# Optimization experiments

Hardware: AMD Instinct MI355X
Metric: run time of the kernel (lower is better)

Reference implementation:

```python
import jax, jax.numpy as jnp
import numpy as np


def setup_inputs() -> dict:
    key = jax.random.key(0)
    k1, k2, k3, k4 = jax.random.split(key, 4)
    N, F, E = 131072, 512, 256
    x = jax.random.normal(k1, (N, F), dtype=jnp.float32)
    W = jax.random.normal(k2, (E, F), dtype=jnp.float32) * 0.05  # stacked weak-classifier weights
    b = jax.random.normal(k3, (E,), dtype=jnp.float32) * 0.05
    alphas = jax.random.normal(k4, (E,), dtype=jnp.float32)
    return {"x": x, "W": W, "b": b, "alphas": alphas}


def reference(x, W, b, alphas):
    # Fused version of the per-estimator Python loop:
    # per estimator e: pred_e = round(sigmoid(x @ W[e] + b[e])) in {0,1}
    logits = jnp.einsum('nf,ef->ne', x, W) + b              # [N, E]
    preds = jnp.round(jax.nn.sigmoid(logits))               # [N, E], half-to-even like torch.round
    # original casts each (alpha * pred) term to long (trunc toward zero) before accumulating
    terms = jnp.trunc(alphas[None, :] * preds)              # [N, E]
    acc = jnp.sum(terms, axis=1)                            # [N]
    return jnp.sign(acc)
```

## Files before the change

### kernel.cpp

```cpp
#include <hip/hip_runtime.h>
#include <math.h>


#define F_DIM 512
#define BM    128
#define BK    32
#define NTMAX 8
#define KPAD  40
#define TAU   1e-3f

typedef float f32x4  __attribute__((ext_vector_type(4)));
typedef short bf16x8 __attribute__((ext_vector_type(8)));
typedef unsigned short u16x4 __attribute__((ext_vector_type(4)));

__device__ inline unsigned short bf16_rne(float v) {
    unsigned u = __float_as_uint(v);
    u += 0x7FFFu + ((u >> 16) & 1u);
    return (unsigned short)(u >> 16);
}
__device__ inline float bf16_to_f32(unsigned short h) {
    return __uint_as_float(((unsigned)h) << 16);
}

__device__ __attribute__((noinline)) bool exact_pred(const float* __restrict__ xr,
                                                     const float* __restrict__ wr,
                                                     float bv) {
    double s0 = 0.0, s1 = 0.0, s2 = 0.0, s3 = 0.0;
    for (int k = 0; k < F_DIM; k += 4) {
        s0 = fma((double)xr[k + 0], (double)wr[k + 0], s0);
        s1 = fma((double)xr[k + 1], (double)wr[k + 1], s1);
        s2 = fma((double)xr[k + 2], (double)wr[k + 2], s2);
        s3 = fma((double)xr[k + 3], (double)wr[k + 3], s3);
    }
    double s = ((s0 + s1) + (s2 + s3)) + (double)bv;
    return s > 0.0;
}

__global__ __launch_bounds__(256, 3)
void ada_mfma(const float* __restrict__ x, const float* __restrict__ W,
              const float* __restrict__ bias, const float* __restrict__ alphas,
              float* __restrict__ out) {
    __shared__ unsigned short xs_hi[BM][KPAD], xs_lo[BM][KPAD];
    __shared__ unsigned short wh[128][KPAD],  wl[128][KPAD];
    __shared__ int   se[272];
    __shared__ float st[272];
    __shared__ float sb[272];
    __shared__ int   wcnt[4];

    const int tid = threadIdx.x;
    const int n0  = blockIdx.x * BM;

    se[tid] = 0; st[tid] = 0.0f; sb[tid] = 0.0f;
    if (tid < 16) { se[256 + tid] = 0; st[256 + tid] = 0.0f; sb[256 + tid] = 0.0f; }
    __syncthreads();
    const float t = truncf(alphas[tid]);
    const bool flag = (t != 0.0f);
    const unsigned long long m64 = __ballot(flag);
    const int lane = tid & 63, wvi = tid >> 6;
    if (lane == 0) wcnt[wvi] = __popcll(m64);
    __syncthreads();
    int off = 0;
    #pragma unroll
    for (int w = 0; w < 4; ++w) if (w < wvi) off += wcnt[w];
    const int M = wcnt[0] + wcnt[1] + wcnt[2] + wcnt[3];
    if (flag) {
        const int slot = off + __popcll(m64 & ((1ull << lane) - 1ull));
        se[slot] = tid; st[slot] = t; sb[slot] = bias[tid];
    }
    __syncthreads();

    const int sr   = tid >> 3;
    const int sc   = (tid & 7) * 4;
    const int quad = (tid >> 4) & 3;
    const int l15  = tid & 15;
    const int rw   = (tid >> 6) * 32;

    const float* xp = x + (size_t)(n0 + sr) * F_DIM + sc;

    int part[2][4];
    #pragma unroll
    for (int mt = 0; mt < 2; ++mt)
        #pragma unroll
        for (int r = 0; r < 4; ++r) part[mt][r] = 0;

    for (int cb = 0; cb < M; cb += 128) {
        const int Mrem   = M - cb;
        const int NT     = (Mrem + 15) >> 4 < NTMAX ? (Mrem + 15) >> 4 : NTMAX;
        const int wstage = (NT + 1) >> 1;

        const float* wp[4];
        #pragma unroll
        for (int i = 0; i < 4; ++i) {
            const int e = se[cb + sr + i * 32];
            wp[i] = W + (size_t)e * F_DIM + sc;
        }

        f32x4 acc[2][NTMAX];
        #pragma unroll
        for (int mt = 0; mt < 2; ++mt)
            #pragma unroll
            for (int nt = 0; nt < NTMAX; ++nt)
                acc[mt][nt] = (f32x4){0.0f, 0.0f, 0.0f, 0.0f};

        for (int k0 = 0; k0 < F_DIM; k0 += BK) {
            float4 xv[4], wvv[4];
            #pragma unroll
            for (int i = 0; i < 4; ++i)
                xv[i] = *(const float4*)(xp + (size_t)i * 32 * F_DIM + k0);
            #pragma unroll
            for (int i = 0; i < 4; ++i)
                if (i < wstage) wvv[i] = *(const float4*)(wp[i] + k0);

            __syncthreads();

            #pragma unroll
            for (int i = 0; i < 4; ++i) {
                const int r = sr + i * 32;
                const float vv[4] = {xv[i].x, xv[i].y, xv[i].z, xv[i].w};
                u16x4 hv, lv;
                #pragma unroll
                for (int j = 0; j < 4; ++j) {
                    const unsigned short h = bf16_rne(vv[j]);
                    hv[j] = h;
                    lv[j] = bf16_rne(vv[j] - bf16_to_f32(h));
                }
                *(u16x4*)&xs_hi[r][sc] = hv;
                *(u16x4*)&xs_lo[r][sc] = lv;
            }
            #pragma unroll
            for (int i = 0; i < 4; ++i) {
                if (i < wstage) {
                    const int r = sr + i * 32;
                    const float vv[4] = {wvv[i].x, wvv[i].y, wvv[i].z, wvv[i].w};
                    u16x4 hv, lv;
                    #pragma unroll
                    for (int j = 0; j < 4; ++j) {
                        const unsigned short h = bf16_rne(vv[j]);
                        hv[j] = h;
                        lv[j] = bf16_rne(vv[j] - bf16_to_f32(h));
                    }
                    *(u16x4*)&wh[r][sc] = hv;
                    *(u16x4*)&wl[r][sc] = lv;
                }
            }

            __syncthreads();

            bf16x8 ah[2], al[2];
            #pragma unroll
            for (int mt = 0; mt < 2; ++mt) {
                ah[mt] = *(const bf16x8*)&xs_hi[rw + mt * 16 + l15][quad * 8];
                al[mt] = *(const bf16x8*)&xs_lo[rw + mt * 16 + l15][quad * 8];
            }
            #pragma unroll
            for (int nt = 0; nt < NTMAX; ++nt) {
                if (nt < NT) {
                    const bf16x8 bh = *(const bf16x8*)&wh[nt * 16 + l15][quad * 8];
                    const bf16x8 bl = *(const bf16x8*)&wl[nt * 16 + l15][quad * 8];
                    #pragma unroll
                    for (int mt = 0; mt < 2; ++mt) {
                        acc[mt][nt] = __builtin_amdgcn_mfma_f32_16x16x32_bf16(ah[mt], bh, acc[mt][nt], 0, 0, 0);
                        acc[mt][nt] = __builtin_amdgcn_mfma_f32_16x16x32_bf16(al[mt], bh, acc[mt][nt], 0, 0, 0);
                        acc[mt][nt] = __builtin_amdgcn_mfma_f32_16x16x32_bf16(ah[mt], bl, acc[mt][nt], 0, 0, 0);
                    }
                }
            }
        }

        #pragma unroll
        for (int nt = 0; nt < NTMAX; ++nt) {
            if (nt < NT) {
                const int col = cb + nt * 16 + l15;
                const float tv = st[col];
                if (tv != 0.0f) {
                    const float bv = sb[col];
                    const int it = (int)tv;
                    #pragma unroll
                    for (int mt = 0; mt < 2; ++mt) {
                        #pragma unroll
                        for (int r = 0; r < 4; ++r) {
                            const float logit = acc[mt][nt][r] + bv;
                            bool pred = (logit > 0.0f);
                            if (fabsf(logit) < TAU) {
                                const int row = rw + mt * 16 + quad * 4 + r;
                                pred = exact_pred(x + (size_t)(n0 + row) * F_DIM,
                                                  W + (size_t)se[col] * F_DIM, bv);
                            }
                            if (pred) part[mt][r] += it;
                        }
                    }
                }
            }
        }
    }

    #pragma unroll
    for (int mt = 0; mt < 2; ++mt) {
        #pragma unroll
        for (int r = 0; r < 4; ++r) {
            int v = part[mt][r];
            v += __shfl_xor(v, 1);
            v += __shfl_xor(v, 2);
            v += __shfl_xor(v, 4);
            v += __shfl_xor(v, 8);
            part[mt][r] = v;
        }
    }
    if (l15 == 0) {
        #pragma unroll
        for (int mt = 0; mt < 2; ++mt) {
            float4 o;
            o.x = (part[mt][0] > 0) ? 1.0f : (part[mt][0] < 0 ? -1.0f : 0.0f);
            o.y = (part[mt][1] > 0) ? 1.0f : (part[mt][1] < 0 ? -1.0f : 0.0f);
            o.z = (part[mt][2] > 0) ? 1.0f : (part[mt][2] < 0 ? -1.0f : 0.0f);
            o.w = (part[mt][3] > 0) ? 1.0f : (part[mt][3] < 0 ? -1.0f : 0.0f);
            *(float4*)(out + n0 + rw + mt * 16 + quad * 4) = o;
        }
    }
}

extern "C" void kernel_launch(void* const* d_in, const int* in_sizes, int n_in,
                              void* d_out, int out_size, void* d_ws, size_t ws_size,
                              hipStream_t stream) {
    const float* x      = (const float*)d_in[0];
    const float* W      = (const float*)d_in[1];
    const float* bias   = (const float*)d_in[2];
    const float* alphas = (const float*)d_in[3];
    float* out = (float*)d_out;

    const int n = in_sizes[0] / F_DIM;
    const int nblocks = n / BM;

    ada_mfma<<<dim3(nblocks), dim3(256), 0, stream>>>(x, W, bias, alphas, out);
}
```

Baseline: 495.2 us.

## Precompute split-bf16 W in workspace and stream operands directly from global to registers

```diff
diff --git a/kernel.cpp b/kernel.cpp
--- a/kernel.cpp
+++ b/kernel.cpp
@@ -3,15 +3,15 @@
 
 
 #define F_DIM 512
-#define BM    128
-#define BK    32
-#define NTMAX 8
-#define KPAD  40
-#define TAU   1e-3f
+#define E_DIM 256
+#define BMROWS 128
+#define CPP    96
+#define NTMAX  6
+#define NSLOT  288
+#define TAU    1e-3f
 
 typedef float f32x4  __attribute__((ext_vector_type(4)));
 typedef short bf16x8 __attribute__((ext_vector_type(8)));
-typedef unsigned short u16x4 __attribute__((ext_vector_type(4)));
 
 __device__ inline unsigned short bf16_rne(float v) {
     unsigned u = __float_as_uint(v);
@@ -20,6 +20,15 @@
 }
 __device__ inline float bf16_to_f32(unsigned short h) {
     return __uint_as_float(((unsigned)h) << 16);
+}
+__device__ inline void cvt8(const float4& a, const float4& b, bf16x8& h8, bf16x8& l8) {
+    const float v[8] = {a.x, a.y, a.z, a.w, b.x, b.y, b.z, b.w};
+    #pragma unroll
+    for (int j = 0; j < 8; ++j) {
+        const unsigned short h = bf16_rne(v[j]);
+        h8[j] = (short)h;
+        l8[j] = (short)bf16_rne(v[j] - bf16_to_f32(h));
+    }
 }
 
 __device__ __attribute__((noinline)) bool exact_pred(const float* __restrict__ xr,
@@ -36,22 +45,62 @@
     return s > 0.0;
 }
 
-__global__ __launch_bounds__(256, 3)
-void ada_mfma(const float* __restrict__ x, const float* __restrict__ W,
+__global__ __launch_bounds__(1024)
+void ada_prep(const float* __restrict__ W, const float* __restrict__ alphas,
+              unsigned short* __restrict__ whi, unsigned short* __restrict__ wlo) {
+    __shared__ int se[NSLOT];
+    __shared__ int wcnt[16];
+
+    const int tid = threadIdx.x;
+    if (tid < NSLOT) se[tid] = -1;
+    if (tid < 16) wcnt[tid] = 0;
+    __syncthreads();
+
+    const bool in_e = (tid < E_DIM);
+    const float t = in_e ? truncf(alphas[tid]) : 0.0f;
+    const bool flag = in_e && (t != 0.0f);
+    const unsigned long long m64 = __ballot(flag);
+    const int lane = tid & 63, wvi = tid >> 6;
+    if (lane == 0) wcnt[wvi] = __popcll(m64);
+    __syncthreads();
+    if (flag) {
+        int off = 0;
+        #pragma unroll
+        for (int w = 0; w < 4; ++w) if (w < wvi) off += wcnt[w];
+        se[off + __popcll(m64 & ((1ull << lane) - 1ull))] = tid;
+    }
+    __syncthreads();
+
+    for (int p = tid; p < NSLOT * (F_DIM / 2); p += 1024) {
+        const int row = p >> 8;
+        const int cp  = (p & 255) * 2;
+        const int e   = se[row];
+        float2 v = make_float2(0.0f, 0.0f);
+        if (e >= 0) v = *(const float2*)(W + (size_t)e * F_DIM + cp);
+        ushort2 h2, l2;
+        h2.x = bf16_rne(v.x); l2.x = bf16_rne(v.x - bf16_to_f32(h2.x));
+        h2.y = bf16_rne(v.y); l2.y = bf16_rne(v.y - bf16_to_f32(h2.y));
+        *(ushort2*)(whi + (size_t)row * F_DIM + cp) = h2;
+        *(ushort2*)(wlo + (size_t)row * F_DIM + cp) = l2;
+    }
+}
+
+template<bool PREW>
+__global__ __launch_bounds__(256)
+void ada_gemm(const float* __restrict__ x, const float* __restrict__ W,
               const float* __restrict__ bias, const float* __restrict__ alphas,
+              const unsigned short* __restrict__ whi,
+              const unsigned short* __restrict__ wlo,
               float* __restrict__ out) {
-    __shared__ unsigned short xs_hi[BM][KPAD], xs_lo[BM][KPAD];
-    __shared__ unsigned short wh[128][KPAD],  wl[128][KPAD];
-    __shared__ int   se[272];
-    __shared__ float st[272];
-    __shared__ float sb[272];
+    __shared__ int   se[NSLOT];
+    __shared__ float st[NSLOT];
+    __shared__ float sb[NSLOT];
     __shared__ int   wcnt[4];
 
     const int tid = threadIdx.x;
-    const int n0  = blockIdx.x * BM;
 
     se[tid] = 0; st[tid] = 0.0f; sb[tid] = 0.0f;
-    if (tid < 16) { se[256 + tid] = 0; st[256 + tid] = 0.0f; sb[256 + tid] = 0.0f; }
+    if (tid < NSLOT - E_DIM) { se[E_DIM + tid] = 0; st[E_DIM + tid] = 0.0f; sb[E_DIM + tid] = 0.0f; }
     __syncthreads();
     const float t = truncf(alphas[tid]);
     const bool flag = (t != 0.0f);
@@ -59,23 +108,21 @@
     const int lane = tid & 63, wvi = tid >> 6;
     if (lane == 0) wcnt[wvi] = __popcll(m64);
     __syncthreads();
-    int off = 0;
-    #pragma unroll
-    for (int w = 0; w < 4; ++w) if (w < wvi) off += wcnt[w];
     const int M = wcnt[0] + wcnt[1] + wcnt[2] + wcnt[3];
     if (flag) {
+        int off = 0;
+        #pragma unroll
+        for (int w = 0; w < 4; ++w) if (w < wvi) off += wcnt[w];
         const int slot = off + __popcll(m64 & ((1ull << lane) - 1ull));
         se[slot] = tid; st[slot] = t; sb[slot] = bias[tid];
     }
     __syncthreads();
 
-    const int sr   = tid >> 3;
-    const int sc   = (tid & 7) * 4;
+    const int l15  = tid & 15;
     const int quad = (tid >> 4) & 3;
-    const int l15  = tid & 15;
-    const int rw   = (tid >> 6) * 32;
-
-    const float* xp = x + (size_t)(n0 + sr) * F_DIM + sc;
+    const int wave = tid >> 6;
+    const int rowbase = blockIdx.x * BMROWS + wave * 32;
+    const float* xrow = x + (size_t)(rowbase + l15) * F_DIM + quad * 8;
 
     int part[2][4];
     #pragma unroll
@@ -83,17 +130,9 @@
         #pragma unroll
         for (int r = 0; r < 4; ++r) part[mt][r] = 0;
 
-    for (int cb = 0; cb < M; cb += 128) {
-        const int Mrem   = M - cb;
-        const int NT     = (Mrem + 15) >> 4 < NTMAX ? (Mrem + 15) >> 4 : NTMAX;
-        const int wstage = (NT + 1) >> 1;
-
-        const float* wp[4];
-        #pragma unroll
-        for (int i = 0; i < 4; ++i) {
-            const int e = se[cb + sr + i * 32];
-            wp[i] = W + (size_t)e * F_DIM + sc;
-        }
+    for (int cb = 0; cb < M; cb += CPP) {
+        const int Mrem = M - cb;
+        const int NT = ((Mrem + 15) >> 4) < NTMAX ? ((Mrem + 15) >> 4) : NTMAX;
 
         f32x4 acc[2][NTMAX];
         #pragma unroll
@@ -102,61 +141,57 @@
             for (int nt = 0; nt < NTMAX; ++nt)
                 acc[mt][nt] = (f32x4){0.0f, 0.0f, 0.0f, 0.0f};
 
-        for (int k0 = 0; k0 < F_DIM; k0 += BK) {
-            float4 xv[4], wvv[4];
-            #pragma unroll
-            for (int i = 0; i < 4; ++i)
-                xv[i] = *(const float4*)(xp + (size_t)i * 32 * F_DIM + k0);
-            #pragma unroll
-            for (int i = 0; i < 4; ++i)
-                if (i < wstage) wvv[i] = *(const float4*)(wp[i] + k0);
-
-            __syncthreads();
-
-            #pragma unroll
-            for (int i = 0; i < 4; ++i) {
-                const int r = sr + i * 32;
-                const float vv[4] = {xv[i].x, xv[i].y, xv[i].z, xv[i].w};
-                u16x4 hv, lv;
+        const unsigned short* bhp[NTMAX];
+        const unsigned short* blp[NTMAX];
+        const float* wrp[NTMAX];
+        #pragma unroll
+        for (int nt = 0; nt < NTMAX; ++nt) {
+            const int col = cb + nt * 16 + l15;
+            if (PREW) {
+                bhp[nt] = whi + (size_t)col * F_DIM + quad * 8;
+                blp[nt] = wlo + (size_t)col * F_DIM + quad * 8;
+            } else {
+                wrp[nt] = W + (size_t)se[col] * F_DIM + quad * 8;
+            }
+        }
+
+        float4 xc0[2], xc1[2];
+        #pragma unroll
+        for (int mt = 0; mt < 2; ++mt) {
+            const float* p = xrow + (size_t)mt * 16 * F_DIM;
+            xc0[mt] = *(const float4*)(p);
+            xc1[mt] = *(const float4*)(p + 4);
+        }
+
+        for (int k0 = 0; k0 < F_DIM; k0 += 32) {
+            float4 xn0[2], xn1[2];
+            const bool more = (k0 + 32) < F_DIM;
+            if (more) {
                 #pragma unroll
-                for (int j = 0; j < 4; ++j) {
-                    const unsigned short h = bf16_rne(vv[j]);
-                    hv[j] = h;
-                    lv[j] = bf16_rne(vv[j] - bf16_to_f32(h));
+                for (int mt = 0; mt < 2; ++mt) {
+                    const float* p = xrow + (size_t)mt * 16 * F_DIM + k0 + 32;
+                    xn0[mt] = *(const float4*)(p);
+                    xn1[mt] = *(const float4*)(p + 4);
                 }
-                *(u16x4*)&xs_hi[r][sc] = hv;
-                *(u16x4*)&xs_lo[r][sc] = lv;
-            }
-            #pragma unroll
-            for (int i = 0; i < 4; ++i) {
-                if (i < wstage) {
-                    const int r = sr + i * 32;
-                    const float vv[4] = {wvv[i].x, wvv[i].y, wvv[i].z, wvv[i].w};
-                    u16x4 hv, lv;
-                    #pragma unroll
-                    for (int j = 0; j < 4; ++j) {
-                        const unsigned short h = bf16_rne(vv[j]);
-                        hv[j] = h;
-                        lv[j] = bf16_rne(vv[j] - bf16_to_f32(h));
-                    }
-                    *(u16x4*)&wh[r][sc] = hv;
-                    *(u16x4*)&wl[r][sc] = lv;
-                }
-            }
-
-            __syncthreads();
+            }
 
             bf16x8 ah[2], al[2];
             #pragma unroll
-            for (int mt = 0; mt < 2; ++mt) {
-                ah[mt] = *(const bf16x8*)&xs_hi[rw + mt * 16 + l15][quad * 8];
-                al[mt] = *(const bf16x8*)&xs_lo[rw + mt * 16 + l15][quad * 8];
-            }
+            for (int mt = 0; mt < 2; ++mt)
+                cvt8(xc0[mt], xc1[mt], ah[mt], al[mt]);
+
             #pragma unroll
             for (int nt = 0; nt < NTMAX; ++nt) {
                 if (nt < NT) {
-                    const bf16x8 bh = *(const bf16x8*)&wh[nt * 16 + l15][quad * 8];
-                    const bf16x8 bl = *(const bf16x8*)&wl[nt * 16 + l15][quad * 8];
+                    bf16x8 bh, bl;
+                    if (PREW) {
+                        bh = *(const bf16x8*)(bhp[nt] + k0);
+                        bl = *(const bf16x8*)(blp[nt] + k0);
+                    } else {
+                        const float4 wa = *(const float4*)(wrp[nt] + k0);
+                        const float4 wb = *(const float4*)(wrp[nt] + k0 + 4);
+                        cvt8(wa, wb, bh, bl);
+                    }
                     #pragma unroll
                     for (int mt = 0; mt < 2; ++mt) {
                         acc[mt][nt] = __builtin_amdgcn_mfma_f32_16x16x32_bf16(ah[mt], bh, acc[mt][nt], 0, 0, 0);
@@ -164,6 +199,11 @@
                         acc[mt][nt] = __builtin_amdgcn_mfma_f32_16x16x32_bf16(ah[mt], bl, acc[mt][nt], 0, 0, 0);
                     }
                 }
+            }
+
+            if (more) {
+                #pragma unroll
+                for (int mt = 0; mt < 2; ++mt) { xc0[mt] = xn0[mt]; xc1[mt] = xn1[mt]; }
             }
         }
 
@@ -182,8 +222,8 @@
                             const float logit = acc[mt][nt][r] + bv;
                             bool pred = (logit > 0.0f);
                             if (fabsf(logit) < TAU) {
-                                const int row = rw + mt * 16 + quad * 4 + r;
-                                pred = exact_pred(x + (size_t)(n0 + row) * F_DIM,
+                                const int grow = rowbase + mt * 16 + quad * 4 + r;
+                                pred = exact_pred(x + (size_t)grow * F_DIM,
                                                   W + (size_t)se[col] * F_DIM, bv);
                             }
                             if (pred) part[mt][r] += it;
@@ -214,7 +254,7 @@
             o.y = (part[mt][1] > 0) ? 1.0f : (part[mt][1] < 0 ? -1.0f : 0.0f);
             o.z = (part[mt][2] > 0) ? 1.0f : (part[mt][2] < 0 ? -1.0f : 0.0f);
             o.w = (part[mt][3] > 0) ? 1.0f : (part[mt][3] < 0 ? -1.0f : 0.0f);
-            *(float4*)(out + n0 + rw + mt * 16 + quad * 4) = o;
+            *(float4*)(out + rowbase + mt * 16 + quad * 4) = o;
         }
     }
 }
@@ -229,7 +269,15 @@
     float* out = (float*)d_out;
 
     const int n = in_sizes[0] / F_DIM;
-    const int nblocks = n / BM;
-
-    ada_mfma<<<dim3(nblocks), dim3(256), 0, stream>>>(x, W, bias, alphas, out);
-}
+    const int nblocks = n / BMROWS;
+
+    const size_t wsneed = (size_t)NSLOT * F_DIM * 2 * sizeof(unsigned short);
+    if (ws_size >= wsneed) {
+        unsigned short* whi = (unsigned short*)d_ws;
+        unsigned short* wlo = whi + (size_t)NSLOT * F_DIM;
+        ada_prep<<<dim3(1), dim3(1024), 0, stream>>>(W, alphas, whi, wlo);
+        ada_gemm<true><<<dim3(nblocks), dim3(256), 0, stream>>>(x, W, bias, alphas, whi, wlo, out);
+    } else {
+        ada_gemm<false><<<dim3(nblocks), dim3(256), 0, stream>>>(x, W, bias, alphas, nullptr, nullptr, out);
+    }
+}
```

Result: slower. 567.4 us (+14.6%).
